# Optimization experiments

Hardware: AMD Instinct MI355X
Metric: run time of the kernel (lower is better)

The kernel has to match this reference:

```python
import jax, jax.numpy as jnp
import numpy as np

MESH_SIZE = 0.01
HID = 256
NUM_RES_LAYERS = 3
TEMP = 1e-3
M_SCALE_LO, M_SCALE_HI = 0.0, 10.0
OFF_LO, OFF_HI = -10.0, 10.0


def _triangle_mesh(step):
    # Preisach triangle: points (beta, alpha) with 0 <= beta <= alpha <= 1
    n = int(round(1.0 / step)) + 1
    g = np.linspace(0.0, 1.0, n).astype(np.float32)
    bb, aa = np.meshgrid(g, g, indexing='ij')
    sel = bb <= aa + 1e-9
    return np.stack([bb[sel], aa[sel]], axis=-1)  # [N, 2] (beta, alpha)


def _glorot(key, shape):
    fan = sum(shape)
    return jax.random.normal(key, shape, dtype=jnp.float32) * np.float32(np.sqrt(2.0 / fan))


def setup_inputs() -> dict:
    key = jax.random.key(0)
    ks = jax.random.split(key, 16)
    B, S, T = 16, 256, 1024
    inp = {
        'encoder_input': jax.random.normal(ks[0], (B, S, 2), dtype=jnp.float32),
        'decoder_input': jax.random.uniform(ks[1], (B, T, 1), dtype=jnp.float32),
        'encoder_mask': jnp.ones((B, S), dtype=jnp.float32),
        'base_mesh': jnp.asarray(_triangle_mesh(MESH_SIZE)),
        # density ResNetMLP params (2 -> HID -> ... -> 1)
        'dens_Win': _glorot(ks[2], (2, HID)),
        'dens_bin': jnp.zeros((HID,), jnp.float32),
        'dens_Wr': _glorot(ks[3], (NUM_RES_LAYERS, HID, HID)),
        'dens_br': jnp.zeros((NUM_RES_LAYERS, HID), jnp.float32),
        'dens_Wout': _glorot(ks[4], (HID, 1)),
        'dens_bout': jnp.zeros((1,), jnp.float32),
        # encoder params: sequence MLP + mesh/context fusion -> initial relay states
        'enc_Ws': _glorot(ks[5], (2, HID)),
        'enc_bs': jnp.zeros((HID,), jnp.float32),
        'enc_Wm': _glorot(ks[6], (3, HID)),
        'enc_Wc': _glorot(ks[7], (HID, HID)),
        'enc_bm': jnp.zeros((HID,), jnp.float32),
        'enc_Wo': _glorot(ks[8], (HID, 1)),
        'enc_bo': jnp.zeros((1,), jnp.float32),
        # constrained scalars (raw, sigmoid-interval transformed)
        'h_scale_raw': jnp.float32(0.0),
        'm_scale_raw': jnp.float32(0.0),
        'm_offset_raw': jnp.float32(0.0),
    }
    return inp


def _interval(raw, lo, hi):
    return lo + (hi - lo) * jax.nn.sigmoid(raw)


def reference(encoder_input, decoder_input, encoder_mask, base_mesh,
              dens_Win, dens_bin, dens_Wr, dens_br, dens_Wout, dens_bout,
              enc_Ws, enc_bs, enc_Wm, enc_Wc, enc_bm, enc_Wo, enc_bo,
              h_scale_raw, m_scale_raw, m_offset_raw):
    B = encoder_input.shape[0]
    mesh = jnp.broadcast_to(base_mesh[None], (B,) + base_mesh.shape)  # [B,N,2]
    # ---- density network (ResNetMLP + sigmoid, eval mode: dropout off)
    x = jax.nn.relu(mesh @ dens_Win + dens_bin)
    def res_block(h, wb):
        w, b = wb
        return h + jax.nn.relu(h @ w + b), None
    x, _ = jax.lax.scan(res_block, x, (dens_Wr, dens_br))
    density = jax.nn.sigmoid(x @ dens_Wout + dens_bout)[..., 0]  # [B,N]
    # ---- encoder: masked mean-pooled sequence context fused with mesh features
    seq = jax.nn.relu(encoder_input @ enc_Ws + enc_bs)  # [B,S,H]
    mask = encoder_mask[..., None]
    ctx = (seq * mask).sum(1) / jnp.maximum(mask.sum(1), 1.0)  # [B,H]
    mesh_feat = jnp.concatenate([mesh, density[..., None]], axis=-1)  # [B,N,3]
    z = jax.nn.relu(mesh_feat @ enc_Wm + (ctx @ enc_Wc)[:, None, :] + enc_bm)
    initial_states = jnp.tanh((z @ enc_Wo + enc_bo)[..., 0])  # [B,N] in [-1,1]
    # ---- soft Preisach relay scan over time
    beta = mesh[..., 0]   # [B,N]
    alpha = mesh[..., 1]  # [B,N]
    h = decoder_input[..., 0]  # [B,T]
    dsum = density.sum(-1)  # [B]
    def relay_step(s, h_t):  # s: [B,N], h_t: [B]
        ht = h_t[:, None]
        w_up = jax.nn.sigmoid((ht - alpha) / TEMP)   # push relay -> +1 when h >= alpha
        w_dn = jax.nn.sigmoid((beta - ht) / TEMP)    # push relay -> -1 when h <= beta
        s = s + w_up * (1.0 - s)
        s = s + w_dn * (-1.0 - s)
        m_t = (density * s).sum(-1) / dsum
        return s, m_t
    _, m_seq = jax.lax.scan(relay_step, initial_states, h.T)  # [T,B]
    m = m_seq.T  # [B,T]
    h_scale = _interval(h_scale_raw, M_SCALE_LO, M_SCALE_HI)
    m_scale = _interval(m_scale_raw, M_SCALE_LO, M_SCALE_HI)
    m_offset = _interval(m_offset_raw, OFF_LO, OFF_HI)
    b_out = h_scale * h + m_scale * m + m_offset
    return (b_out, density, m, initial_states, mesh)
```

## Files before the change

kernel.cpp:

```cpp
#include <hip/hip_runtime.h>
#include <hip/hip_bf16.h>
#include <math.h>

constexpr int kB = 16;
constexpr int kS = 256;
constexpr int kT = 1024;
constexpr int kM = 5151;
constexpr int kH = 256;
constexpr int kG = 16;
constexpr int kL = 64;
constexpr int kJW = 84;
constexpr float kSig = 1442.6950408889634f;
constexpr float kAiS = 14.426950408889634f;

constexpr int OFF_BOUT = 0;
constexpr int OFF_DENS = kB * kT;
constexpr int OFF_M    = OFF_DENS + kB * kM;
constexpr int OFF_IS   = OFF_M + kB * kT;
constexpr int OFF_MESH = OFF_IS + kB * kM;

constexpr int WS_TAB  = 0;
constexpr int WS_X1   = 851968;
constexpr int WS_X2   = 2170624;
constexpr int WS_ISF  = 3489280;
constexpr int WS_PART = 3571712;
constexpr int WS_DENS = 4259840;
constexpr int WS_DENSP= 4265216;

__device__ __forceinline__ float exp2_fast(float x){ return __builtin_amdgcn_exp2f(x); }
__device__ __forceinline__ float rcp_fast(float x){ return __builtin_amdgcn_rcpf(x); }
__device__ __forceinline__ void wave_lds_fence(){
    asm volatile("s_waitcnt lgkmcnt(0)" ::: "memory");
}

__global__ __launch_bounds__(256) void k_tab(const float* __restrict__ dec,
        __hip_bfloat16* __restrict__ TAB, float* __restrict__ dens_pre){
    int t  = blockIdx.x * 256 + threadIdx.x;
    int ai = blockIdx.y;
    int b  = blockIdx.z;
    if (ai == 0 && b == 0){
        for (int i = t; i < 5376; i += 1024) dens_pre[i] = 0.f;
    }
    float hts = dec[b * kT + t] * kSig;
    float wu = rcp_fast(1.f + exp2_fast(fmaf((float)ai, kAiS, -hts)));
    TAB[(size_t)(b * 101 + ai) * kT + t] = __float2bfloat16(wu);
}

__global__ __launch_bounds__(256) void k_res_first(const float* __restrict__ mesh,
        const float* __restrict__ Win, const float* __restrict__ bin,
        const float* __restrict__ Wl, const float* __restrict__ bl,
        float* __restrict__ xout){
    __shared__ float xT[64 * 34];
    __shared__ float Wsh[64 * 64];
    __shared__ float beL[32], alL[32];
    int tid = threadIdx.x;
    int og = tid & 31, pg = tid >> 5;
    int jb = blockIdx.x * 32;
    int ob = blockIdx.y * 64;
    if (tid < 32){
        int jg = jb + tid;
        beL[tid] = (jg < kM) ? mesh[2*jg]   : 0.f;
        alL[tid] = (jg < kM) ? mesh[2*jg+1] : 0.f;
    }
    __syncthreads();
    float acc[4][2] = {};
    int ks = tid & 63;
    int j0 = tid >> 6;
    for (int sl = 0; sl < 4; ++sl){
        int kb = sl * 64;
        float w0k = Win[kb + ks], w1k = Win[kH + kb + ks], bk = bin[kb + ks];
        #pragma unroll
        for (int it = 0; it < 8; ++it){
            int j = j0 + it * 4;
            xT[ks * 34 + j] = fmaxf(fmaf(beL[j], w0k, fmaf(alL[j], w1k, bk)), 0.f);
        }
        #pragma unroll
        for (int it = 0; it < 16; ++it){
            int idx = tid + it * 256;
            int o = idx & 63, k = idx >> 6;
            Wsh[k * 64 + o] = Wl[(kb + k) * kH + ob + o];
        }
        __syncthreads();
        #pragma unroll 4
        for (int k = 0; k < 64; ++k){
            float2 x01 = *(const float2*)&xT[k * 34 + pg * 4];
            float2 x23 = *(const float2*)&xT[k * 34 + pg * 4 + 2];
            float w0 = Wsh[k * 64 + og];
            float w1 = Wsh[k * 64 + og + 32];
            acc[0][0] = fmaf(x01.x, w0, acc[0][0]); acc[0][1] = fmaf(x01.x, w1, acc[0][1]);
            acc[1][0] = fmaf(x01.y, w0, acc[1][0]); acc[1][1] = fmaf(x01.y, w1, acc[1][1]);
            acc[2][0] = fmaf(x23.x, w0, acc[2][0]); acc[2][1] = fmaf(x23.x, w1, acc[2][1]);
            acc[3][0] = fmaf(x23.y, w0, acc[3][0]); acc[3][1] = fmaf(x23.y, w1, acc[3][1]);
        }
        __syncthreads();
    }
    #pragma unroll
    for (int i = 0; i < 4; ++i){
        int jl = pg * 4 + i;
        int jg = jb + jl;
        if (jg >= kM) continue;
        float be = beL[jl], al = alL[jl];
        #pragma unroll
        for (int r = 0; r < 2; ++r){
            int o = ob + og + 32 * r;
            float x0v = fmaxf(fmaf(be, Win[o], fmaf(al, Win[kH + o], bin[o])), 0.f);
            float v = acc[i][r] + bl[o];
            xout[jg * kH + o] = x0v + fmaxf(v, 0.f);
        }
    }
}

template<bool kDOT>
__global__ __launch_bounds__(256) void k_res_t(const float* __restrict__ xin,
        const float* __restrict__ Wl, const float* __restrict__ bl,
        float* __restrict__ xout, const float* __restrict__ Wout,
        float* __restrict__ dens_pre){
    __shared__ float xT[64 * 34];
    __shared__ float Wsh[64 * 64];
    int tid = threadIdx.x;
    int og = tid & 31, pg = tid >> 5;
    int jb = blockIdx.x * 32;
    int ob = blockIdx.y * 64;
    float acc[4][2] = {};
    int ks = tid & 63;
    int j0 = tid >> 6;
    for (int sl = 0; sl < 4; ++sl){
        int kb = sl * 64;
        #pragma unroll
        for (int it = 0; it < 8; ++it){
            int j = j0 + it * 4;
            int jg = jb + j;
            xT[ks * 34 + j] = (jg < kM) ? xin[jg * kH + kb + ks] : 0.f;
        }
        #pragma unroll
        for (int it = 0; it < 16; ++it){
            int idx = tid + it * 256;
            int o = idx & 63, k = idx >> 6;
            Wsh[k * 64 + o] = Wl[(kb + k) * kH + ob + o];
        }
        __syncthreads();
        #pragma unroll 4
        for (int k = 0; k < 64; ++k){
            float2 x01 = *(const float2*)&xT[k * 34 + pg * 4];
            float2 x23 = *(const float2*)&xT[k * 34 + pg * 4 + 2];
            float w0 = Wsh[k * 64 + og];
            float w1 = Wsh[k * 64 + og + 32];
            acc[0][0] = fmaf(x01.x, w0, acc[0][0]); acc[0][1] = fmaf(x01.x, w1, acc[0][1]);
            acc[1][0] = fmaf(x01.y, w0, acc[1][0]); acc[1][1] = fmaf(x01.y, w1, acc[1][1]);
            acc[2][0] = fmaf(x23.x, w0, acc[2][0]); acc[2][1] = fmaf(x23.x, w1, acc[2][1]);
            acc[3][0] = fmaf(x23.y, w0, acc[3][0]); acc[3][1] = fmaf(x23.y, w1, acc[3][1]);
        }
        __syncthreads();
    }
    float wo0 = 0.f, wo1 = 0.f;
    if (kDOT){ wo0 = Wout[ob + og]; wo1 = Wout[ob + og + 32]; }
    #pragma unroll
    for (int i = 0; i < 4; ++i){
        int jg = jb + pg * 4 + i;
        float v0 = 0.f, v1 = 0.f;
        if (jg < kM){
            float a0 = acc[i][0] + bl[ob + og];
            float a1 = acc[i][1] + bl[ob + og + 32];
            v0 = xin[jg * kH + ob + og]      + fmaxf(a0, 0.f);
            v1 = xin[jg * kH + ob + og + 32] + fmaxf(a1, 0.f);
            if (!kDOT){
                xout[jg * kH + ob + og]      = v0;
                xout[jg * kH + ob + og + 32] = v1;
            }
        }
        if (kDOT){
            float p = fmaf(v0, wo0, v1 * wo1);
            p += __shfl_down(p, 16, 64);
            p += __shfl_down(p, 8, 64);
            p += __shfl_down(p, 4, 64);
            p += __shfl_down(p, 2, 64);
            p += __shfl_down(p, 1, 64);
            if (og == 0 && jg < kM) atomicAdd(&dens_pre[jg], p);
        }
    }
}

__global__ __launch_bounds__(256) void k_init(const float* __restrict__ enc_in,
        const float* __restrict__ mask, const float* __restrict__ Ws,
        const float* __restrict__ bs, const float* __restrict__ Wc,
        const float* __restrict__ mesh, const float* __restrict__ dens_pre,
        const float* __restrict__ bout, const float* __restrict__ Wm,
        const float* __restrict__ bm, const float* __restrict__ Wo,
        const float* __restrict__ bo, float* __restrict__ dens,
        float* __restrict__ isf, float* __restrict__ out){
    __shared__ float ctx_l[kH];
    __shared__ float w0s[kH], w1s[kH], w2s[kH], bcs[kH], wos[kH];
    int tid = threadIdx.x;
    int b = blockIdx.y;
    {
        float w0 = Ws[tid], w1 = Ws[kH + tid], bh = bs[tid];
        float acc = 0.f, msum = 0.f;
        const float* e = enc_in + b * kS * 2;
        const float* mk = mask + b * kS;
        #pragma unroll 4
        for (int s = 0; s < kS; ++s){
            float e0 = e[2*s], e1 = e[2*s+1], mm = mk[s];
            float v = fmaxf(fmaf(e0, w0, fmaf(e1, w1, bh)), 0.f);
            acc = fmaf(v, mm, acc);
            msum += mm;
        }
        ctx_l[tid] = acc / fmaxf(msum, 1.f);
    }
    __syncthreads();
    float cw = 0.f;
    #pragma unroll 8
    for (int k = 0; k < kH; ++k) cw = fmaf(ctx_l[k], Wc[k * kH + tid], cw);
    w0s[tid] = Wm[tid];
    w1s[tid] = Wm[kH + tid];
    w2s[tid] = Wm[2*kH + tid];
    bcs[tid] = bm[tid] + cw;
    wos[tid] = Wo[tid];
    __syncthreads();
    int j = blockIdx.x * 256 + tid;
    if (j >= kM) return;
    float d = 1.f / (1.f + expf(-(dens_pre[j] + bout[0])));
    if (b == 0) dens[j] = d;
    float be = mesh[2*j], al = mesh[2*j+1];
    float acc = 0.f;
    #pragma unroll 8
    for (int h = 0; h < kH; ++h){
        float pre = fmaf(be, w0s[h], fmaf(al, w1s[h], fmaf(d, w2s[h], bcs[h])));
        acc = fmaf(fmaxf(pre, 0.f), wos[h], acc);
    }
    float s = tanhf(acc + bo[0]);
    isf[b * kM + j] = s;
    out[OFF_IS + b * kM + j] = s;
}

__device__ __forceinline__ float bfhalf(unsigned int w, int odd){
    return __uint_as_float(odd ? (w & 0xffff0000u) : (w << 16));
}

__global__ __launch_bounds__(64) void k_scan(const float* __restrict__ mesh,
        const float* __restrict__ dens, const float* __restrict__ isf,
        const __hip_bfloat16* __restrict__ TAB,
        __hip_bfloat16* __restrict__ partials, float* __restrict__ out){
    __shared__ unsigned short cb[kL * 66];
    int L = threadIdx.x;
    int blk = blockIdx.x;
    int xcd = blk & 7;
    int i   = blk >> 3;
    int b   = (xcd << 1) | (i >= kJW ? 1 : 0);
    int jw  = (i >= kJW) ? i - kJW : i;
    int j = jw * 64 + L;
    bool valid = j < kM;
    int jj = valid ? j : 0;
    float d  = valid ? dens[j] : 0.f;
    float q  = valid ? isf[b * kM + j] + 1.f : 0.f;
    float be = mesh[2*jj], al = mesh[2*jj+1];
    int ai = __float2int_rn(al * 100.f);
    int bi = __float2int_rn(be * 100.f);
    const __hip_bfloat16* ra = TAB + (size_t)(b * 101 + ai) * kT;
    const __hip_bfloat16* rb = TAB + (size_t)(b * 101 + bi) * kT;
    if (valid){
        out[OFF_DENS + b * kM + j] = d;
        out[OFF_MESH + 2 * (b * kM + j)]     = be;
        out[OFF_MESH + 2 * (b * kM + j) + 1] = al;
    }
    size_t pbase = (size_t)(b * kJW + jw) * kT + L;

    unsigned int uaA[32], ubA[32], uaB[32], ubB[32];

    auto load_chunk = [&](int g, unsigned int* UA, unsigned int* UB){
        const uint4* pa = (const uint4*)(ra + g * kL);
        const uint4* pb = (const uint4*)(rb + g * kL);
        #pragma unroll
        for (int i2 = 0; i2 < 8; ++i2){
            uint4 va = pa[i2];
            UA[4*i2]=va.x; UA[4*i2+1]=va.y; UA[4*i2+2]=va.z; UA[4*i2+3]=va.w;
        }
        #pragma unroll
        for (int i2 = 0; i2 < 8; ++i2){
            uint4 vb = pb[i2];
            UB[4*i2]=vb.x; UB[4*i2+1]=vb.y; UB[4*i2+2]=vb.z; UB[4*i2+3]=vb.w;
        }
    };
    auto compute_chunk = [&](int g, const unsigned int* UA, const unsigned int* UB){
        #pragma unroll
        for (int t = 0; t < kL; ++t){
            float u = bfhalf(UA[t>>1], t & 1);
            float w = bfhalf(UB[t>>1], t & 1);
            q = w * fmaf(u, 2.f - q, q);
            float v = fmaf(d, q, -d);
            cb[t * 66 + L] = (unsigned short)(__float_as_uint(v) >> 16);
        }
        wave_lds_fence();
        float a0 = 0.f, a1 = 0.f;
        const __hip_bfloat162* row = (const __hip_bfloat162*)&cb[L * 66];
        #pragma unroll
        for (int i2 = 0; i2 < 32; ++i2){
            float2 f = __bfloat1622float2(row[i2]);
            a0 += f.x; a1 += f.y;
        }
        partials[pbase + g * kL] = __float2bfloat16(a0 + a1);
        wave_lds_fence();
    };

    load_chunk(0, uaA, ubA);
    #pragma unroll 1
    for (int g = 0; g < kG; g += 2){
        load_chunk(g + 1, uaB, ubB);
        compute_chunk(g, uaA, ubA);
        if (g + 2 < kG) load_chunk(g + 2, uaA, ubA);
        compute_chunk(g + 1, uaB, ubB);
    }
}

__global__ __launch_bounds__(256) void k_final(const __hip_bfloat16* __restrict__ partials,
        const float* __restrict__ dens, const float* __restrict__ dec,
        const float* __restrict__ hsr, const float* __restrict__ msr,
        const float* __restrict__ mor, float* __restrict__ out){
    __shared__ float red[4];
    int tid = threadIdx.x;
    int b = blockIdx.y;
    float ds = 0.f;
    for (int i = tid; i < kM; i += 256) ds += dens[i];
    #pragma unroll
    for (int off = 32; off; off >>= 1) ds += __shfl_down(ds, off, 64);
    if ((tid & 63) == 0) red[tid >> 6] = ds;
    __syncthreads();
    float dsum = red[0] + red[1] + red[2] + red[3];
    int t = blockIdx.x * 256 + tid;
    float acc = 0.f;
    const __hip_bfloat16* p = partials + (size_t)b * kJW * kT + t;
    #pragma unroll 4
    for (int w = 0; w < kJW; ++w) acc += __bfloat162float(p[(size_t)w * kT]);
    float m = acc / dsum;
    float hscale = 10.f / (1.f + expf(-hsr[0]));
    float mscale = 10.f / (1.f + expf(-msr[0]));
    float moff   = -10.f + 20.f / (1.f + expf(-mor[0]));
    float h = dec[b * kT + t];
    out[OFF_M + b * kT + t]    = m;
    out[OFF_BOUT + b * kT + t] = fmaf(hscale, h, fmaf(mscale, m, moff));
}

extern "C" void kernel_launch(void* const* d_in, const int* in_sizes, int n_in,
                              void* d_out, int out_size, void* d_ws, size_t ws_size,
                              hipStream_t stream) {
    (void)in_sizes; (void)n_in; (void)out_size; (void)ws_size;
    const float* enc_in = (const float*)d_in[0];
    const float* dec    = (const float*)d_in[1];
    const float* mask   = (const float*)d_in[2];
    const float* mesh   = (const float*)d_in[3];
    const float* Win    = (const float*)d_in[4];
    const float* bin    = (const float*)d_in[5];
    const float* Wr     = (const float*)d_in[6];
    const float* br     = (const float*)d_in[7];
    const float* Wout   = (const float*)d_in[8];
    const float* bout   = (const float*)d_in[9];
    const float* Ws     = (const float*)d_in[10];
    const float* bs     = (const float*)d_in[11];
    const float* Wm     = (const float*)d_in[12];
    const float* Wc     = (const float*)d_in[13];
    const float* bm     = (const float*)d_in[14];
    const float* Wo     = (const float*)d_in[15];
    const float* bo     = (const float*)d_in[16];
    const float* hsr    = (const float*)d_in[17];
    const float* msr    = (const float*)d_in[18];
    const float* mor    = (const float*)d_in[19];
    float* out = (float*)d_out;

    float* ws = (float*)d_ws;
    __hip_bfloat16* TAB      = (__hip_bfloat16*)(ws + WS_TAB);
    float* x1    = ws + WS_X1;
    float* x2    = ws + WS_X2;
    float* isf   = ws + WS_ISF;
    __hip_bfloat16* partials = (__hip_bfloat16*)(ws + WS_PART);
    float* densv = ws + WS_DENS;
    float* densp = ws + WS_DENSP;

    k_tab         <<<dim3(4, 101, kB),  256, 0, stream>>>(dec, TAB, densp);
    k_res_first   <<<dim3(161, 4),      256, 0, stream>>>(mesh, Win, bin, Wr, br, x1);
    k_res_t<false><<<dim3(161, 4),      256, 0, stream>>>(x1, Wr + 65536,  br + 256, x2, nullptr, nullptr);
    k_res_t<true> <<<dim3(161, 4),      256, 0, stream>>>(x2, Wr + 131072, br + 512, nullptr, Wout, densp);
    k_init        <<<dim3(21, kB),      256, 0, stream>>>(enc_in, mask, Ws, bs, Wc, mesh, densp,
                                                          bout, Wm, bm, Wo, bo, densv, isf, out);
    k_scan        <<<dim3(kJW * kB),     64, 0, stream>>>(mesh, densv, isf, TAB, partials, out);
    k_final       <<<dim3(4, kB),       256, 0, stream>>>(partials, densv, dec, hsr, msr, mor, out);
}
```

Measured before the change: 248.1 us.

## Fuse three density ResNet layers into one kernel keeping activations in LDS

Replaces the three separate residual-layer kernels, which each wrote a 5151x256 activation matrix to global memory, with one kernel. Each block keeps a 16-point activation tile resident in shared memory across all three layers and streams the weight matrices through shared memory. The output dot product is reduced in shared memory and written directly, removing the atomics and the zeroing pass. In exchange each block re-reads all weights, and the grid drops to 322 blocks, which lowers parallelism.

After: 246.5 us. Within noise of the previous version (-0.6%).

```diff
diff --git a/kernel.cpp b/kernel.cpp
--- a/kernel.cpp
+++ b/kernel.cpp
@@ -10,6 +10,8 @@
 constexpr int kG = 16;
 constexpr int kL = 64;
 constexpr int kJW = 84;
+constexpr int kJT = 16;
+constexpr int kRB = 322;
 constexpr float kSig = 1442.6950408889634f;
 constexpr float kAiS = 14.426950408889634f;
 
@@ -20,8 +22,6 @@
 constexpr int OFF_MESH = OFF_IS + kB * kM;
 
 constexpr int WS_TAB  = 0;
-constexpr int WS_X1   = 851968;
-constexpr int WS_X2   = 2170624;
 constexpr int WS_ISF  = 3489280;
 constexpr int WS_PART = 3571712;
 constexpr int WS_DENS = 4259840;
@@ -34,149 +34,86 @@
 }
 
 __global__ __launch_bounds__(256) void k_tab(const float* __restrict__ dec,
-        __hip_bfloat16* __restrict__ TAB, float* __restrict__ dens_pre){
+        __hip_bfloat16* __restrict__ TAB){
     int t  = blockIdx.x * 256 + threadIdx.x;
     int ai = blockIdx.y;
     int b  = blockIdx.z;
-    if (ai == 0 && b == 0){
-        for (int i = t; i < 5376; i += 1024) dens_pre[i] = 0.f;
-    }
     float hts = dec[b * kT + t] * kSig;
     float wu = rcp_fast(1.f + exp2_fast(fmaf((float)ai, kAiS, -hts)));
     TAB[(size_t)(b * 101 + ai) * kT + t] = __float2bfloat16(wu);
 }
 
-__global__ __launch_bounds__(256) void k_res_first(const float* __restrict__ mesh,
+__global__ __launch_bounds__(256) void k_res3(const float* __restrict__ mesh,
         const float* __restrict__ Win, const float* __restrict__ bin,
-        const float* __restrict__ Wl, const float* __restrict__ bl,
-        float* __restrict__ xout){
-    __shared__ float xT[64 * 34];
-    __shared__ float Wsh[64 * 64];
-    __shared__ float beL[32], alL[32];
-    int tid = threadIdx.x;
-    int og = tid & 31, pg = tid >> 5;
-    int jb = blockIdx.x * 32;
-    int ob = blockIdx.y * 64;
-    if (tid < 32){
-        int jg = jb + tid;
-        beL[tid] = (jg < kM) ? mesh[2*jg]   : 0.f;
-        alL[tid] = (jg < kM) ? mesh[2*jg+1] : 0.f;
-    }
-    __syncthreads();
-    float acc[4][2] = {};
-    int ks = tid & 63;
-    int j0 = tid >> 6;
-    for (int sl = 0; sl < 4; ++sl){
-        int kb = sl * 64;
-        float w0k = Win[kb + ks], w1k = Win[kH + kb + ks], bk = bin[kb + ks];
-        #pragma unroll
-        for (int it = 0; it < 8; ++it){
-            int j = j0 + it * 4;
-            xT[ks * 34 + j] = fmaxf(fmaf(beL[j], w0k, fmaf(alL[j], w1k, bk)), 0.f);
-        }
-        #pragma unroll
-        for (int it = 0; it < 16; ++it){
-            int idx = tid + it * 256;
-            int o = idx & 63, k = idx >> 6;
-            Wsh[k * 64 + o] = Wl[(kb + k) * kH + ob + o];
+        const float* __restrict__ Wr, const float* __restrict__ br,
+        const float* __restrict__ Wout, float* __restrict__ dens_pre){
+    __shared__ float xL[256 * 16];
+    __shared__ float Wsh[32 * 256];
+    __shared__ float dred[256];
+    __shared__ float beL[16], alL[16];
+    int t = threadIdx.x;
+    int jl = t & 15, oo = t >> 4;
+    int jb = blockIdx.x * kJT;
+    if (t < 16){
+        int jg = jb + t;
+        beL[t] = (jg < kM) ? mesh[2*jg]   : 0.f;
+        alL[t] = (jg < kM) ? mesh[2*jg+1] : 0.f;
+    }
+    __syncthreads();
+    #pragma unroll
+    for (int it = 0; it < 16; ++it){
+        int lin = t + it * 256;
+        int k = lin >> 4, j = lin & 15;
+        xL[lin] = fmaxf(fmaf(beL[j], Win[k], fmaf(alL[j], Win[kH + k], bin[k])), 0.f);
+    }
+    for (int l = 0; l < 3; ++l){
+        const float* W  = Wr + l * kH * kH;
+        const float* bl = br + l * kH;
+        float acc[16] = {};
+        for (int ks = 0; ks < 8; ++ks){
+            __syncthreads();
+            const float4* Wg = (const float4*)(W + ks * 32 * kH);
+            float4* Ws4 = (float4*)Wsh;
+            #pragma unroll
+            for (int it = 0; it < 8; ++it) Ws4[t + it * 256] = Wg[t + it * 256];
+            __syncthreads();
+            #pragma unroll 2
+            for (int k = 0; k < 32; ++k){
+                float xv = xL[(ks * 32 + k) * 16 + jl];
+                const float4* wrow = (const float4*)&Wsh[k * 256 + oo * 16];
+                float4 w0 = wrow[0], w1 = wrow[1], w2 = wrow[2], w3 = wrow[3];
+                acc[ 0] = fmaf(xv, w0.x, acc[ 0]); acc[ 1] = fmaf(xv, w0.y, acc[ 1]);
+                acc[ 2] = fmaf(xv, w0.z, acc[ 2]); acc[ 3] = fmaf(xv, w0.w, acc[ 3]);
+                acc[ 4] = fmaf(xv, w1.x, acc[ 4]); acc[ 5] = fmaf(xv, w1.y, acc[ 5]);
+                acc[ 6] = fmaf(xv, w1.z, acc[ 6]); acc[ 7] = fmaf(xv, w1.w, acc[ 7]);
+                acc[ 8] = fmaf(xv, w2.x, acc[ 8]); acc[ 9] = fmaf(xv, w2.y, acc[ 9]);
+                acc[10] = fmaf(xv, w2.z, acc[10]); acc[11] = fmaf(xv, w2.w, acc[11]);
+                acc[12] = fmaf(xv, w3.x, acc[12]); acc[13] = fmaf(xv, w3.y, acc[13]);
+                acc[14] = fmaf(xv, w3.z, acc[14]); acc[15] = fmaf(xv, w3.w, acc[15]);
+            }
         }
         __syncthreads();
-        #pragma unroll 4
-        for (int k = 0; k < 64; ++k){
-            float2 x01 = *(const float2*)&xT[k * 34 + pg * 4];
-            float2 x23 = *(const float2*)&xT[k * 34 + pg * 4 + 2];
-            float w0 = Wsh[k * 64 + og];
-            float w1 = Wsh[k * 64 + og + 32];
-            acc[0][0] = fmaf(x01.x, w0, acc[0][0]); acc[0][1] = fmaf(x01.x, w1, acc[0][1]);
-            acc[1][0] = fmaf(x01.y, w0, acc[1][0]); acc[1][1] = fmaf(x01.y, w1, acc[1][1]);
-            acc[2][0] = fmaf(x23.x, w0, acc[2][0]); acc[2][1] = fmaf(x23.x, w1, acc[2][1]);
-            acc[3][0] = fmaf(x23.y, w0, acc[3][0]); acc[3][1] = fmaf(x23.y, w1, acc[3][1]);
-        }
-        __syncthreads();
-    }
+        #pragma unroll
+        for (int i = 0; i < 16; ++i){
+            int o = oo * 16 + i;
+            float xo = xL[o * 16 + jl];
+            xL[o * 16 + jl] = xo + fmaxf(acc[i] + bl[o], 0.f);
+        }
+    }
+    float p = 0.f;
     #pragma unroll
-    for (int i = 0; i < 4; ++i){
-        int jl = pg * 4 + i;
-        int jg = jb + jl;
-        if (jg >= kM) continue;
-        float be = beL[jl], al = alL[jl];
-        #pragma unroll
-        for (int r = 0; r < 2; ++r){
-            int o = ob + og + 32 * r;
-            float x0v = fmaxf(fmaf(be, Win[o], fmaf(al, Win[kH + o], bin[o])), 0.f);
-            float v = acc[i][r] + bl[o];
-            xout[jg * kH + o] = x0v + fmaxf(v, 0.f);
-        }
-    }
-}
-
-template<bool kDOT>
-__global__ __launch_bounds__(256) void k_res_t(const float* __restrict__ xin,
-        const float* __restrict__ Wl, const float* __restrict__ bl,
-        float* __restrict__ xout, const float* __restrict__ Wout,
-        float* __restrict__ dens_pre){
-    __shared__ float xT[64 * 34];
-    __shared__ float Wsh[64 * 64];
-    int tid = threadIdx.x;
-    int og = tid & 31, pg = tid >> 5;
-    int jb = blockIdx.x * 32;
-    int ob = blockIdx.y * 64;
-    float acc[4][2] = {};
-    int ks = tid & 63;
-    int j0 = tid >> 6;
-    for (int sl = 0; sl < 4; ++sl){
-        int kb = sl * 64;
-        #pragma unroll
-        for (int it = 0; it < 8; ++it){
-            int j = j0 + it * 4;
-            int jg = jb + j;
-            xT[ks * 34 + j] = (jg < kM) ? xin[jg * kH + kb + ks] : 0.f;
-        }
-        #pragma unroll
-        for (int it = 0; it < 16; ++it){
-            int idx = tid + it * 256;
-            int o = idx & 63, k = idx >> 6;
-            Wsh[k * 64 + o] = Wl[(kb + k) * kH + ob + o];
-        }
-        __syncthreads();
-        #pragma unroll 4
-        for (int k = 0; k < 64; ++k){
-            float2 x01 = *(const float2*)&xT[k * 34 + pg * 4];
-            float2 x23 = *(const float2*)&xT[k * 34 + pg * 4 + 2];
-            float w0 = Wsh[k * 64 + og];
-            float w1 = Wsh[k * 64 + og + 32];
-            acc[0][0] = fmaf(x01.x, w0, acc[0][0]); acc[0][1] = fmaf(x01.x, w1, acc[0][1]);
-            acc[1][0] = fmaf(x01.y, w0, acc[1][0]); acc[1][1] = fmaf(x01.y, w1, acc[1][1]);
-            acc[2][0] = fmaf(x23.x, w0, acc[2][0]); acc[2][1] = fmaf(x23.x, w1, acc[2][1]);
-            acc[3][0] = fmaf(x23.y, w0, acc[3][0]); acc[3][1] = fmaf(x23.y, w1, acc[3][1]);
-        }
-        __syncthreads();
-    }
-    float wo0 = 0.f, wo1 = 0.f;
-    if (kDOT){ wo0 = Wout[ob + og]; wo1 = Wout[ob + og + 32]; }
-    #pragma unroll
-    for (int i = 0; i < 4; ++i){
-        int jg = jb + pg * 4 + i;
-        float v0 = 0.f, v1 = 0.f;
-        if (jg < kM){
-            float a0 = acc[i][0] + bl[ob + og];
-            float a1 = acc[i][1] + bl[ob + og + 32];
-            v0 = xin[jg * kH + ob + og]      + fmaxf(a0, 0.f);
-            v1 = xin[jg * kH + ob + og + 32] + fmaxf(a1, 0.f);
-            if (!kDOT){
-                xout[jg * kH + ob + og]      = v0;
-                xout[jg * kH + ob + og + 32] = v1;
-            }
-        }
-        if (kDOT){
-            float p = fmaf(v0, wo0, v1 * wo1);
-            p += __shfl_down(p, 16, 64);
-            p += __shfl_down(p, 8, 64);
-            p += __shfl_down(p, 4, 64);
-            p += __shfl_down(p, 2, 64);
-            p += __shfl_down(p, 1, 64);
-            if (og == 0 && jg < kM) atomicAdd(&dens_pre[jg], p);
-        }
+    for (int i = 0; i < 16; ++i){
+        int o = oo * 16 + i;
+        p = fmaf(xL[o * 16 + jl], Wout[o], p);
+    }
+    dred[t] = p;
+    __syncthreads();
+    if (t < 16){
+        float s = 0.f;
+        #pragma unroll
+        for (int ii = 0; ii < 16; ++ii) s += dred[ii * 16 + t];
+        int jg = jb + t;
+        if (jg < kM) dens_pre[jg] = s;
     }
 }
 
@@ -367,19 +304,15 @@
 
     float* ws = (float*)d_ws;
     __hip_bfloat16* TAB      = (__hip_bfloat16*)(ws + WS_TAB);
-    float* x1    = ws + WS_X1;
-    float* x2    = ws + WS_X2;
     float* isf   = ws + WS_ISF;
     __hip_bfloat16* partials = (__hip_bfloat16*)(ws + WS_PART);
     float* densv = ws + WS_DENS;
     float* densp = ws + WS_DENSP;
 
-    k_tab         <<<dim3(4, 101, kB),  256, 0, stream>>>(dec, TAB, densp);
-    k_res_first   <<<dim3(161, 4),      256, 0, stream>>>(mesh, Win, bin, Wr, br, x1);
-    k_res_t<false><<<dim3(161, 4),      256, 0, stream>>>(x1, Wr + 65536,  br + 256, x2, nullptr, nullptr);
-    k_res_t<true> <<<dim3(161, 4),      256, 0, stream>>>(x2, Wr + 131072, br + 512, nullptr, Wout, densp);
-    k_init        <<<dim3(21, kB),      256, 0, stream>>>(enc_in, mask, Ws, bs, Wc, mesh, densp,
-                                                          bout, Wm, bm, Wo, bo, densv, isf, out);
-    k_scan        <<<dim3(kJW * kB),     64, 0, stream>>>(mesh, densv, isf, TAB, partials, out);
-    k_final       <<<dim3(4, kB),       256, 0, stream>>>(partials, densv, dec, hsr, msr, mor, out);
-}
+    k_tab   <<<dim3(4, 101, kB),  256, 0, stream>>>(dec, TAB);
+    k_res3  <<<dim3(kRB),         256, 0, stream>>>(mesh, Win, bin, Wr, br, Wout, densp);
+    k_init  <<<dim3(21, kB),      256, 0, stream>>>(enc_in, mask, Ws, bs, Wc, mesh, densp,
+                                                    bout, Wm, bm, Wo, bo, densv, isf, out);
+    k_scan  <<<dim3(kJW * kB),     64, 0, stream>>>(mesh, densv, isf, TAB, partials, out);
+    k_final <<<dim3(4, kB),       256, 0, stream>>>(partials, densv, dec, hsr, msr, mor, out);
+}
```
